# Kernel tuning notes

Hardware: AMD Instinct MI355X
Metric: run time of the kernel (lower is better)

The kernel has to match this reference:

```python
import jax, jax.numpy as jnp
import numpy as np

B = 64        # number of graph segments
BASE = 384    # mean verts per segment
LMAX = 512    # pad length (counts in [256, 512])
H_DIM = 256
H_DIV = 128   # h_dim // h_dim_div
HEADS = 4
DH = H_DIV // HEADS  # 32


def _counts(seed):
    rng = np.random.default_rng(seed)
    d = rng.integers(-128, 129, B)
    d[1::2] = -d[::2]            # paired so the total is exactly B*BASE
    return (BASE + d).astype(np.int64)


def _pad_indices(counts, L):
    # Gather indices/mask mapping packed ragged tokens -> padded [B, L].
    counts = np.asarray(counts)
    off = np.concatenate([[0], np.cumsum(counts)[:-1]])
    ar = np.arange(L)[None, :]
    mask = ar < counts[:, None]
    idx = np.where(mask, off[:, None] + ar, 0)
    return idx, mask


def setup_inputs() -> dict:
    key = jax.random.key(0)
    ks = jax.random.split(key, 16)
    src_num_verts = _counts(0)
    dst_num_verts = _counts(1)
    total = B * BASE  # 24576 for both src and dst

    def w(k, shape):
        return 0.02 * jax.random.normal(k, shape, jnp.float32)

    return {
        'src_h': jax.random.normal(ks[0], (total, H_DIM), jnp.float32),
        'dst_h': jax.random.normal(ks[1], (total, H_DIM), jnp.float32),
        'src_num_verts': src_num_verts,
        'dst_num_verts': dst_num_verts,
        # 1x1 Conv1d == linear over channels
        'Wq': w(ks[2], (H_DIV, H_DIM)), 'bq': w(ks[3], (H_DIV,)),
        'Wk': w(ks[4], (H_DIV, H_DIM)), 'bk': w(ks[5], (H_DIV,)),
        'Wv': w(ks[6], (H_DIV, H_DIM)), 'bv': w(ks[7], (H_DIV,)),
        'Wm': w(ks[8], (H_DIV, H_DIV)), 'bm': w(ks[9], (H_DIV,)),
        'W1': w(ks[10], (H_DIM, H_DIM + H_DIV)), 'b1': w(ks[11], (H_DIM,)),
        'g1': 1.0 + 0.1 * jax.random.normal(ks[12], (H_DIM,), jnp.float32),
        'be1': w(ks[13], (H_DIM,)),
        'rm1': w(ks[14], (H_DIM,)),
        'rv1': jax.random.uniform(ks[15], (H_DIM,), jnp.float32, 0.5, 1.5),
        'W2': w(jax.random.fold_in(key, 100), (H_DIM, H_DIM)),
        'b2': w(jax.random.fold_in(key, 101), (H_DIM,)),
        'g2': 1.0 + 0.1 * jax.random.normal(jax.random.fold_in(key, 102), (H_DIM,), jnp.float32),
        'be2': w(jax.random.fold_in(key, 103), (H_DIM,)),
        'rm2': w(jax.random.fold_in(key, 104), (H_DIM,)),
        'rv2': jax.random.uniform(jax.random.fold_in(key, 105), (H_DIM,), jnp.float32, 0.5, 1.5),
    }


def _bn(x, g, b, rm, rv):
    # BatchNorm1d in eval mode (running stats)
    return (x - rm) / jnp.sqrt(rv + 1e-5) * g + b


def reference(src_h, dst_h, src_num_verts, dst_num_verts,
              Wq, bq, Wk, bk, Wv, bv, Wm, bm,
              W1, b1, g1, be1, rm1, rv1,
              W2, b2, g2, be2, rm2, rv2):
    didx, dmask = _pad_indices(dst_num_verts, LMAX)
    sidx, smask = _pad_indices(src_num_verts, LMAX)

    # fused projections over all packed tokens (1x1 conv == matmul)
    q = src_h_proj = dst_h @ Wq.T + bq        # [Nd, H_DIV]
    k = src_h @ Wk.T + bk                     # [Ns, H_DIV]
    v = src_h @ Wv.T + bv

    # pad to block-diagonal batched form; channel c = d*HEADS + h per torch view
    qp = q[didx].reshape(B, LMAX, DH, HEADS)
    kp = k[sidx].reshape(B, LMAX, DH, HEADS)
    vp = v[sidx].reshape(B, LMAX, DH, HEADS)

    scores = jnp.einsum('bndh,bmdh->bhnm', qp, kp) / (DH ** 0.5)
    scores = jnp.where(jnp.asarray(smask)[:, None, None, :], scores, -1e9)
    attn = jax.nn.softmax(scores, axis=-1)
    msg = jnp.einsum('bhnm,bmdh->bndh', attn, vp).reshape(B, LMAX, H_DIV)
    msg = msg @ Wm.T + bm                     # merge conv

    bb, ii = np.nonzero(dmask)                # unpad back to packed layout
    h_msg = msg[bb, ii]                       # [Nd, H_DIV]

    x = jnp.concatenate([dst_h, h_msg], axis=-1)
    x = _bn(x @ W1.T + b1, g1, be1, rm1, rv1)
    x = jax.nn.relu(x)
    x = _bn(x @ W2.T + b2, g2, be2, rm2, rv2)
    return dst_h + x
```

## Files before the change

kernel.cpp:

```cpp
#include <hip/hip_runtime.h>
#include <hip/hip_bf16.h>
#include <math.h>

#define B_SEG 64
#define HDIM 256
#define HDIV 128
#define NHEADS 4
#define DH 32
#define QSC 0.17677669529663687f

typedef unsigned short u16;
typedef unsigned int u32;

typedef __attribute__((ext_vector_type(8))) short s8v;
typedef __attribute__((ext_vector_type(4))) short s4v;
typedef __attribute__((ext_vector_type(4))) float f4v;

#if defined(__HIP_DEVICE_COMPILE__)
#if __has_builtin(__builtin_amdgcn_mfma_f32_16x16x16_bf16)
#define MFMA16(a, b, c) __builtin_amdgcn_mfma_f32_16x16x16_bf16(a, b, c, 0, 0, 0)
#elif __has_builtin(__builtin_amdgcn_mfma_f32_16x16x16bf16_1k)
#define MFMA16(a, b, c) __builtin_amdgcn_mfma_f32_16x16x16bf16_1k(a, b, c, 0, 0, 0)
#else
#error "no 16x16x16 bf16 mfma builtin on device"
#endif
#else
#define MFMA16(a, b, c) (c)
#endif

__device__ __forceinline__ u16 f2bf(float f) {
    u32 v;
    __builtin_memcpy(&v, &f, 4);
    u32 r = v + 0x7fffu + ((v >> 16) & 1u);
    return (u16)(r >> 16);
}

__device__ __forceinline__ void async_cp16(const u16* g, u16* l) {
    __builtin_amdgcn_global_load_lds(
        (const __attribute__((address_space(1))) u32*)g,
        (__attribute__((address_space(3))) u32*)l, 16, 0, 0);
}

__global__ __launch_bounds__(256) void k_prep(
    const float* __restrict__ Wq, const float* __restrict__ bq,
    const float* __restrict__ Wk, const float* __restrict__ bk,
    const float* __restrict__ Wv, const float* __restrict__ bv,
    const float* __restrict__ Wm, const float* __restrict__ bm,
    const float* __restrict__ W1, const float* __restrict__ b1,
    const float* __restrict__ g1, const float* __restrict__ be1,
    const float* __restrict__ rm1, const float* __restrict__ rv1,
    const float* __restrict__ W2, const float* __restrict__ b2,
    const float* __restrict__ g2, const float* __restrict__ be2,
    const float* __restrict__ rm2, const float* __restrict__ rv2,
    const int* __restrict__ sc_raw, const int* __restrict__ dc_raw,
    const float* __restrict__ src_h, const float* __restrict__ dst_h,
    int* __restrict__ meta,
    u16* __restrict__ pWq, u16* __restrict__ pWkv,
    u16* __restrict__ pW1f, u16* __restrict__ pW2,
    float* __restrict__ bqp, float* __restrict__ bkvp,
    float* __restrict__ sc1, float* __restrict__ sh1,
    float* __restrict__ sc2, float* __restrict__ sh2,
    u16* __restrict__ srcb, u16* __restrict__ dstb, int ntot) {
    if (blockIdx.x < 1028) {
        int idx = blockIdx.x * 256 + threadIdx.x;
        if (idx < 32768) {
            int cp = idx >> 8, k = idx & 255;
            int c = ((cp & 31) << 2) | (cp >> 5);
            pWq[idx] = f2bf(Wq[c * 256 + k]);
        } else if (idx < 98304) {
            int i = idx - 32768;
            int rp = i >> 8, k = i & 255;
            int r = rp & 127;
            int c = ((r & 31) << 2) | (r >> 5);
            float v = (rp < 128) ? Wk[c * 256 + k] : Wv[c * 256 + k];
            pWkv[i] = f2bf(v);
        } else if (idx < 163840) {
            int i = idx - 98304;
            int o = i >> 8, k = i & 255;
            pW1f[o * 384 + k] = f2bf(W1[o * 384 + k]);
        } else if (idx < 196608) {
            int i = idx - 163840;
            int o = i >> 7, cp = i & 127;
            int c = ((cp & 31) << 2) | (cp >> 5);
            float acc = 0.f;
            for (int j = 0; j < 128; j++)
                acc += W1[o * 384 + 256 + j] * Wm[j * 128 + c];
            pW1f[o * 384 + 256 + cp] = f2bf(acc);
        } else if (idx < 262144) {
            int i = idx - 196608;
            pW2[i] = f2bf(W2[i]);
        } else if (idx < 263168) {
            int p = idx - 262144;
            if (p < 128) {
                int c = ((p & 31) << 2) | (p >> 5);
                bqp[p] = bq[c] * QSC;
            } else if (p < 384) {
                int r = p - 128; int rr = r & 127;
                int c = ((rr & 31) << 2) | (rr >> 5);
                bkvp[r] = (r < 128) ? bk[c] : bv[c];
            } else if (p < 640) {
                int o = p - 384;
                float bsum = 0.f;
                for (int j = 0; j < 128; j++)
                    bsum += W1[o * 384 + 256 + j] * bm[j];
                float s = g1[o] * rsqrtf(rv1[o] + 1e-5f);
                sc1[o] = s;
                sh1[o] = (b1[o] + bsum - rm1[o]) * s + be1[o];
            } else if (p < 896) {
                int o = p - 640;
                float s = g2[o] * rsqrtf(rv2[o] + 1e-5f);
                sc2[o] = s;
                sh2[o] = (b2[o] - rm2[o]) * s + be2[o];
            }
        }
    } else if (blockIdx.x == 1028) {
        if (threadIdx.x == 0) {
            bool is64 = (sc_raw[1] == 0);
            int so = 0, dofs = 0;
            for (int i = 0; i < B_SEG; i++) {
                int s = is64 ? sc_raw[2 * i] : sc_raw[i];
                int d = is64 ? dc_raw[2 * i] : dc_raw[i];
                meta[i] = s; meta[64 + i] = d;
                meta[128 + i] = so; meta[192 + i] = dofs;
                so += s; dofs += d;
            }
        }
    } else {
        int i = (blockIdx.x - 1029) * 256 + threadIdx.x;
        int half = ntot * 64;
        const float4* s;
        u16* o;
        int j = i;
        if (i < half) { s = (const float4*)src_h; o = srcb; }
        else { s = (const float4*)dst_h; o = dstb; j = i - half; }
        float4 v = s[j];
        ushort4 u = {f2bf(v.x), f2bf(v.y), f2bf(v.z), f2bf(v.w)};
        ((ushort4*)o)[j] = u;
    }
}

__device__ __forceinline__ void gemm_body(
    const u16* __restrict__ A, int lda,
    const u16* __restrict__ A2, int lda2, int K1,
    const u16* __restrict__ Bw, int K, int m0, int n0,
    const float* __restrict__ scale, const float* __restrict__ shift,
    const float* __restrict__ resid,
    void* __restrict__ Cout, int ldc, int flags,
    u16* Al, u16* Bl) {
    int tid = threadIdx.x;
    int w = tid >> 6, lane = tid & 63;
    int wm = w & 1, wn = w >> 1;
    int l15 = lane & 15, quad = lane >> 4;
    int srow = w * 32 + (lane >> 2);
    int scol = (lane & 3) << 3;
    u16* al0 = Al + w * 1024;
    u16* bl0 = Bl + w * 1024;
    f4v acc[4][4] = {};

    for (int k0 = 0; k0 < K; k0 += 32) {
        const u16* Ag; int aL, acol;
        if (k0 < K1) { Ag = A; aL = lda; acol = k0; }
        else { Ag = A2; aL = lda2; acol = k0 - K1; }
        async_cp16(&Ag[(size_t)(m0 + srow) * aL + acol + scol], al0);
        async_cp16(&Ag[(size_t)(m0 + srow + 16) * aL + acol + scol], al0 + 512);
        async_cp16(&Bw[(size_t)(n0 + srow) * K + k0 + scol], bl0);
        async_cp16(&Bw[(size_t)(n0 + srow + 16) * K + k0 + scol], bl0 + 512);
        __syncthreads();
        s8v af[4], bf[4];
#pragma unroll
        for (int i = 0; i < 4; i++)
            af[i] = *(const s8v*)(&Al[(wm * 64 + i * 16 + l15) * 32 + quad * 8]);
#pragma unroll
        for (int j = 0; j < 4; j++)
            bf[j] = *(const s8v*)(&Bl[(wn * 64 + j * 16 + l15) * 32 + quad * 8]);
#pragma unroll
        for (int i = 0; i < 4; i++)
#pragma unroll
            for (int j = 0; j < 4; j++)
                acc[i][j] = __builtin_amdgcn_mfma_f32_16x16x32_bf16(
                    af[i], bf[j], acc[i][j], 0, 0, 0);
        __syncthreads();
    }
#pragma unroll
    for (int i = 0; i < 4; i++) {
#pragma unroll
        for (int j = 0; j < 4; j++) {
            int n = n0 + wn * 64 + j * 16 + l15;
            float sc = scale ? scale[n] : 1.f;
            float sh = shift ? shift[n] : 0.f;
#pragma unroll
            for (int r = 0; r < 4; r++) {
                int m = m0 + wm * 64 + i * 16 + quad * 4 + r;
                float v = acc[i][j][r];
                if (flags & 4) v *= QSC;
                v = v * sc + sh;
                if (flags & 1) v = fmaxf(v, 0.f);
                if (resid) v += resid[(size_t)m * 256 + n];
                if (flags & 2) ((float*)Cout)[(size_t)m * ldc + n] = v;
                else ((u16*)Cout)[(size_t)m * ldc + n] = f2bf(v);
            }
        }
    }
}

__global__ __launch_bounds__(256) void k_qkv(
    const u16* __restrict__ dstb, const u16* __restrict__ srcb,
    const u16* __restrict__ pWq, const u16* __restrict__ pWkv,
    const float* __restrict__ bqp, const float* __restrict__ bkvp,
    u16* __restrict__ qb, u16* __restrict__ kvb) {
    __shared__ u16 Al[4096];
    __shared__ u16 Bl[4096];
    int m0 = blockIdx.x * 128;
    if (blockIdx.y == 0)
        gemm_body(dstb, 256, dstb, 256, 256, pWq, 256, m0, 0,
                  nullptr, bqp, nullptr, qb, 128, 4, Al, Bl);
    else
        gemm_body(srcb, 256, srcb, 256, 256, pWkv, 256, m0, (blockIdx.y - 1) * 128,
                  nullptr, bkvp, nullptr, kvb, 256, 0, Al, Bl);
}

__global__ __launch_bounds__(256, 4) void k_mlp(
    const u16* __restrict__ dstb, const u16* __restrict__ msgb,
    const u16* __restrict__ pW1f, const u16* __restrict__ pW2,
    const float* __restrict__ sc1, const float* __restrict__ sh1,
    const float* __restrict__ sc2, const float* __restrict__ sh2,
    const float* __restrict__ dst_h, float* __restrict__ out) {
    __shared__ u16 Al[32 * 32];
    __shared__ u16 Bl[256 * 32];
    __shared__ u16 X1[32 * 256];
    int m0 = blockIdx.x * 32;
    int tid = threadIdx.x;
    int w = tid >> 6, lane = tid & 63;
    int l15 = lane & 15, quad = lane >> 4;
    int srow = lane >> 2;
    int scol = (lane & 3) << 3;
    f4v acc[2][4];

#pragma unroll
    for (int i = 0; i < 2; i++)
#pragma unroll
        for (int j = 0; j < 4; j++) acc[i][j] = (f4v){0.f, 0.f, 0.f, 0.f};

    for (int k0 = 0; k0 < 384; k0 += 32) {
        const u16* Ag; int aL, acol;
        if (k0 < 256) { Ag = dstb; aL = 256; acol = k0; }
        else { Ag = msgb; aL = 128; acol = k0 - 256; }
#pragma unroll
        for (int q = 0; q < 4; q++)
            async_cp16(&pW1f[(size_t)(w * 64 + q * 16 + srow) * 384 + k0 + scol],
                       Bl + (w * 64 + q * 16) * 32);
        if (w < 2)
            async_cp16(&Ag[(size_t)(m0 + w * 16 + srow) * aL + acol + scol],
                       Al + w * 16 * 32);
        __syncthreads();
        s8v af[2], bf[4];
#pragma unroll
        for (int i = 0; i < 2; i++)
            af[i] = *(const s8v*)(&Al[(i * 16 + l15) * 32 + quad * 8]);
#pragma unroll
        for (int j = 0; j < 4; j++)
            bf[j] = *(const s8v*)(&Bl[(w * 64 + j * 16 + l15) * 32 + quad * 8]);
#pragma unroll
        for (int i = 0; i < 2; i++)
#pragma unroll
            for (int j = 0; j < 4; j++)
                acc[i][j] = __builtin_amdgcn_mfma_f32_16x16x32_bf16(
                    af[i], bf[j], acc[i][j], 0, 0, 0);
        __syncthreads();
    }
#pragma unroll
    for (int i = 0; i < 2; i++) {
#pragma unroll
        for (int j = 0; j < 4; j++) {
            int n = w * 64 + j * 16 + l15;
            float sc = sc1[n], sh = sh1[n];
#pragma unroll
            for (int r = 0; r < 4; r++) {
                int row = i * 16 + quad * 4 + r;
                float v = fmaxf(acc[i][j][r] * sc + sh, 0.f);
                X1[row * 256 + ((n >> 3) ^ (row & 7)) * 8 + (n & 7)] = f2bf(v);
            }
        }
    }
    __syncthreads();

#pragma unroll
    for (int i = 0; i < 2; i++)
#pragma unroll
        for (int j = 0; j < 4; j++) acc[i][j] = (f4v){0.f, 0.f, 0.f, 0.f};

    for (int k0 = 0; k0 < 256; k0 += 32) {
#pragma unroll
        for (int q = 0; q < 4; q++)
            async_cp16(&pW2[(size_t)(w * 64 + q * 16 + srow) * 256 + k0 + scol],
                       Bl + (w * 64 + q * 16) * 32);
        __syncthreads();
        s8v af[2], bf[4];
#pragma unroll
        for (int i = 0; i < 2; i++) {
            int row = i * 16 + l15;
            af[i] = *(const s8v*)(
                &X1[row * 256 + (((k0 >> 3) + quad) ^ (row & 7)) * 8]);
        }
#pragma unroll
        for (int j = 0; j < 4; j++)
            bf[j] = *(const s8v*)(&Bl[(w * 64 + j * 16 + l15) * 32 + quad * 8]);
#pragma unroll
        for (int i = 0; i < 2; i++)
#pragma unroll
            for (int j = 0; j < 4; j++)
                acc[i][j] = __builtin_amdgcn_mfma_f32_16x16x32_bf16(
                    af[i], bf[j], acc[i][j], 0, 0, 0);
        __syncthreads();
    }
#pragma unroll
    for (int i = 0; i < 2; i++) {
#pragma unroll
        for (int j = 0; j < 4; j++) {
            int n = w * 64 + j * 16 + l15;
            float sc = sc2[n], sh = sh2[n];
#pragma unroll
            for (int r = 0; r < 4; r++) {
                int m = m0 + i * 16 + quad * 4 + r;
                float v = acc[i][j][r] * sc + sh + dst_h[(size_t)m * 256 + n];
                out[(size_t)m * 256 + n] = v;
            }
        }
    }
}

__global__ __launch_bounds__(512, 4) void k_attn(
    const u16* __restrict__ qb, const u16* __restrict__ kvb,
    const int* __restrict__ meta, u16* __restrict__ msgb) {
    extern __shared__ u16 sm[];
    u16* Kl = sm;
    u16* Vl = sm + 16384;
    int b = blockIdx.x, h = blockIdx.y, z = blockIdx.z;
    int ns = meta[b], nd = meta[64 + b];
    int soff = meta[128 + b], doff = meta[192 + b];
    int tid = threadIdx.x, w = tid >> 6, lane = tid & 63;
    int l15 = lane & 15, quad = lane >> 4;

    {
        int m = tid;
        if (m < ns) {
            const uint4* ks = (const uint4*)&kvb[(size_t)(soff + m) * 256 + h * 32];
#pragma unroll
            for (int s = 0; s < 4; s++)
                *(uint4*)&Kl[m * 32 + (s ^ ((m >> 1) & 3)) * 8] = ks[s];
            uint4 vv[4];
            const uint4* vs =
                (const uint4*)&kvb[(size_t)(soff + m) * 256 + 128 + h * 32];
#pragma unroll
            for (int s = 0; s < 4; s++) vv[s] = vs[s];
            const u16* pv = (const u16*)vv;
#pragma unroll
            for (int d = 0; d < 32; d++)
                Vl[d * 512 + ((m >> 3) ^ (d & 7)) * 8 + (m & 7)] = pv[d];
        } else {
#pragma unroll
            for (int d = 0; d < 32; d++)
                Vl[d * 512 + ((m >> 3) ^ (d & 7)) * 8 + (m & 7)] = 0;
        }
    }
    __syncthreads();

    int nc32 = (ns + 31) >> 5;
    int ksw = (quad ^ ((l15 >> 1) & 3)) * 8;
    int vsw = l15 & 7;
    int half4 = (quad & 1) * 4;
    const u16* VlLo = Vl + l15 * 512;
    const u16* VlHi = Vl + (16 + l15) * 512;

    for (int s0 = (z * 8 + w) * 16; s0 < nd; s0 += 256) {
        int qr = min(s0 + l15, nd - 1);
        s8v aq = *(const s8v*)&qb[(size_t)(doff + qr) * 128 + h * 32 + quad * 8];

        f4v oa0 = {0.f, 0.f, 0.f, 0.f};
        f4v oa1 = {0.f, 0.f, 0.f, 0.f};
        float lsum = 0.f;
        for (int c = 0; c < nc32; c++) {
            int kr0 = c * 32 + l15;
            s8v bk0 = *(const s8v*)&Kl[kr0 * 32 + ksw];
            s8v bk1 = *(const s8v*)&Kl[(kr0 + 16) * 32 + ksw];
            f4v sa = __builtin_amdgcn_mfma_f32_16x16x32_bf16(
                bk0, aq, (f4v){0.f, 0.f, 0.f, 0.f}, 0, 0, 0);
            f4v sb = __builtin_amdgcn_mfma_f32_16x16x32_bf16(
                bk1, aq, (f4v){0.f, 0.f, 0.f, 0.f}, 0, 0, 0);
            int kb = c * 32 + quad * 4;
            float e0[4], e1[4];
#pragma unroll
            for (int r = 0; r < 4; r++) {
                float va = (kb + r < ns) ? __expf(sa[r]) : 0.f;
                float vb = (kb + 16 + r < ns) ? __expf(sb[r]) : 0.f;
                e0[r] = va; e1[r] = vb;
                lsum += va + vb;
            }
            union { s4v v; u32 u[2]; } pb0, pb1;
            pb0.u[0] = (u32)f2bf(e0[0]) | ((u32)f2bf(e0[1]) << 16);
            pb0.u[1] = (u32)f2bf(e0[2]) | ((u32)f2bf(e0[3]) << 16);
            pb1.u[0] = (u32)f2bf(e1[0]) | ((u32)f2bf(e1[1]) << 16);
            pb1.u[1] = (u32)f2bf(e1[2]) | ((u32)f2bf(e1[3]) << 16);
            int slb = c * 4 + (quad >> 1);
            s4v v00 = *(const s4v*)&VlLo[(slb ^ vsw) * 8 + half4];
            s4v v01 = *(const s4v*)&VlLo[((slb + 2) ^ vsw) * 8 + half4];
            s4v v10 = *(const s4v*)&VlHi[(slb ^ vsw) * 8 + half4];
            s4v v11 = *(const s4v*)&VlHi[((slb + 2) ^ vsw) * 8 + half4];
            oa0 = MFMA16(v00, pb0.v, oa0);
            oa0 = MFMA16(v01, pb1.v, oa0);
            oa1 = MFMA16(v10, pb0.v, oa1);
            oa1 = MFMA16(v11, pb1.v, oa1);
        }
        lsum += __shfl_xor(lsum, 16, 64);
        lsum += __shfl_xor(lsum, 32, 64);
        float inv = 1.f / lsum;
        int row = s0 + l15;
        if (row < nd) {
            size_t base = (size_t)(doff + row) * 128 + h * 32;
            ushort4 o0 = {f2bf(oa0[0] * inv), f2bf(oa0[1] * inv),
                          f2bf(oa0[2] * inv), f2bf(oa0[3] * inv)};
            ushort4 o1 = {f2bf(oa1[0] * inv), f2bf(oa1[1] * inv),
                          f2bf(oa1[2] * inv), f2bf(oa1[3] * inv)};
            *(ushort4*)&msgb[base + quad * 4] = o0;
            *(ushort4*)&msgb[base + 16 + quad * 4] = o1;
        }
    }
}

extern "C" void kernel_launch(void* const* d_in, const int* in_sizes, int n_in,
                              void* d_out, int out_size, void* d_ws, size_t ws_size,
                              hipStream_t stream) {
    const float* src_h = (const float*)d_in[0];
    const float* dst_h = (const float*)d_in[1];
    const int* snv = (const int*)d_in[2];
    const int* dnv = (const int*)d_in[3];
    const float* Wq = (const float*)d_in[4];  const float* bq = (const float*)d_in[5];
    const float* Wk = (const float*)d_in[6];  const float* bk = (const float*)d_in[7];
    const float* Wv = (const float*)d_in[8];  const float* bv = (const float*)d_in[9];
    const float* Wm = (const float*)d_in[10]; const float* bm = (const float*)d_in[11];
    const float* W1 = (const float*)d_in[12]; const float* b1 = (const float*)d_in[13];
    const float* g1 = (const float*)d_in[14]; const float* be1 = (const float*)d_in[15];
    const float* rm1 = (const float*)d_in[16]; const float* rv1 = (const float*)d_in[17];
    const float* W2 = (const float*)d_in[18]; const float* b2 = (const float*)d_in[19];
    const float* g2 = (const float*)d_in[20]; const float* be2 = (const float*)d_in[21];
    const float* rm2 = (const float*)d_in[22]; const float* rv2 = (const float*)d_in[23];

    int ntot = out_size / HDIM;
    int mt = ntot / 128;

    char* ws = (char*)d_ws;
    int* meta = (int*)ws;
    float* bqp = (float*)(ws + 4096);
    float* bkvp = (float*)(ws + 4608);
    float* sc1 = (float*)(ws + 6144);
    float* sh1 = (float*)(ws + 7168);
    float* sc2 = (float*)(ws + 8192);
    float* sh2 = (float*)(ws + 9216);
    u16* pWq = (u16*)(ws + 16384);
    u16* pWkv = (u16*)(ws + 81920);
    u16* pW1f = (u16*)(ws + 212992);
    u16* pW2 = (u16*)(ws + 409600);
    u16* srcb = (u16*)(ws + 1048576);
    u16* dstb = (u16*)(ws + 13631488);
    u16* msgb = (u16*)(ws + 26214400);

    u16* qb = (u16*)d_out;
    u16* kvb = qb + (size_t)ntot * 128;

    (void)hipFuncSetAttribute((const void*)k_attn,
                              hipFuncAttributeMaxDynamicSharedMemorySize, 65536);

    k_prep<<<dim3(1029 + ntot / 2), dim3(256), 0, stream>>>(
        Wq, bq, Wk, bk, Wv, bv, Wm, bm, W1, b1, g1, be1, rm1, rv1,
        W2, b2, g2, be2, rm2, rv2, snv, dnv, src_h, dst_h, meta,
        pWq, pWkv, pW1f, pW2, bqp, bkvp, sc1, sh1, sc2, sh2,
        srcb, dstb, ntot);
    k_qkv<<<dim3(mt, 3), dim3(256), 0, stream>>>(
        dstb, srcb, pWq, pWkv, bqp, bkvp, qb, kvb);
    k_attn<<<dim3(B_SEG, NHEADS, 2), dim3(512), 65536, stream>>>(
        qb, kvb, meta, msgb);
    k_mlp<<<dim3(ntot / 32), dim3(256), 0, stream>>>(
        dstb, msgb, pW1f, pW2, sc1, sh1, sc2, sh2, dst_h, (float*)d_out);
}
```

Before: 203.2 us.

## Double-buffer LDS tiles in the QKV and MLP GEMM loops

Adds ping-pong shared-memory buffers to the QKV projection GEMM and to both GEMM phases of the fused MLP kernel. The next K-slice is issued with async copies before the MFMAs on the current slice, so global-load latency can overlap with compute, and one barrier per iteration is removed. The first W2 slice is also prefetched while the first layer's epilogue runs. In exchange, LDS use grows, to about 52KB per block in k_mlp, which may lower the number of resident blocks below the requested 4.

Result: no change. 201.2 us (-1.0%).

```diff
diff --git a/kernel.cpp b/kernel.cpp
--- a/kernel.cpp
+++ b/kernel.cpp
@@ -153,26 +153,34 @@
     int l15 = lane & 15, quad = lane >> 4;
     int srow = w * 32 + (lane >> 2);
     int scol = (lane & 3) << 3;
-    u16* al0 = Al + w * 1024;
-    u16* bl0 = Bl + w * 1024;
     f4v acc[4][4] = {};
 
-    for (int k0 = 0; k0 < K; k0 += 32) {
+    auto STAGE = [&](int buf, int k0) {
         const u16* Ag; int aL, acol;
         if (k0 < K1) { Ag = A; aL = lda; acol = k0; }
         else { Ag = A2; aL = lda2; acol = k0 - K1; }
+        u16* al0 = Al + buf * 4096 + w * 1024;
+        u16* bl0 = Bl + buf * 4096 + w * 1024;
         async_cp16(&Ag[(size_t)(m0 + srow) * aL + acol + scol], al0);
         async_cp16(&Ag[(size_t)(m0 + srow + 16) * aL + acol + scol], al0 + 512);
         async_cp16(&Bw[(size_t)(n0 + srow) * K + k0 + scol], bl0);
         async_cp16(&Bw[(size_t)(n0 + srow + 16) * K + k0 + scol], bl0 + 512);
-        __syncthreads();
+    };
+
+    STAGE(0, 0);
+    __syncthreads();
+    int cur = 0;
+    for (int k0 = 0; k0 < K; k0 += 32) {
+        if (k0 + 32 < K) STAGE(cur ^ 1, k0 + 32);
+        const u16* Ab = Al + cur * 4096;
+        const u16* Bb = Bl + cur * 4096;
         s8v af[4], bf[4];
 #pragma unroll
         for (int i = 0; i < 4; i++)
-            af[i] = *(const s8v*)(&Al[(wm * 64 + i * 16 + l15) * 32 + quad * 8]);
+            af[i] = *(const s8v*)(&Ab[(wm * 64 + i * 16 + l15) * 32 + quad * 8]);
 #pragma unroll
         for (int j = 0; j < 4; j++)
-            bf[j] = *(const s8v*)(&Bl[(wn * 64 + j * 16 + l15) * 32 + quad * 8]);
+            bf[j] = *(const s8v*)(&Bb[(wn * 64 + j * 16 + l15) * 32 + quad * 8]);
 #pragma unroll
         for (int i = 0; i < 4; i++)
 #pragma unroll
@@ -180,6 +188,7 @@
                 acc[i][j] = __builtin_amdgcn_mfma_f32_16x16x32_bf16(
                     af[i], bf[j], acc[i][j], 0, 0, 0);
         __syncthreads();
+        cur ^= 1;
     }
 #pragma unroll
     for (int i = 0; i < 4; i++) {
@@ -208,8 +217,8 @@
     const u16* __restrict__ pWq, const u16* __restrict__ pWkv,
     const float* __restrict__ bqp, const float* __restrict__ bkvp,
     u16* __restrict__ qb, u16* __restrict__ kvb) {
-    __shared__ u16 Al[4096];
-    __shared__ u16 Bl[4096];
+    __shared__ u16 Al[8192];
+    __shared__ u16 Bl[8192];
     int m0 = blockIdx.x * 128;
     if (blockIdx.y == 0)
         gemm_body(dstb, 256, dstb, 256, 256, pWq, 256, m0, 0,
@@ -225,8 +234,8 @@
     const float* __restrict__ sc1, const float* __restrict__ sh1,
     const float* __restrict__ sc2, const float* __restrict__ sh2,
     const float* __restrict__ dst_h, float* __restrict__ out) {
-    __shared__ u16 Al[32 * 32];
-    __shared__ u16 Bl[256 * 32];
+    __shared__ u16 Al[2048];
+    __shared__ u16 Bl[16384];
     __shared__ u16 X1[32 * 256];
     int m0 = blockIdx.x * 32;
     int tid = threadIdx.x;
@@ -236,30 +245,44 @@
     int scol = (lane & 3) << 3;
     f4v acc[2][4];
 
-#pragma unroll
-    for (int i = 0; i < 2; i++)
-#pragma unroll
-        for (int j = 0; j < 4; j++) acc[i][j] = (f4v){0.f, 0.f, 0.f, 0.f};
-
-    for (int k0 = 0; k0 < 384; k0 += 32) {
+    auto STAGE1 = [&](int buf, int k0) {
         const u16* Ag; int aL, acol;
         if (k0 < 256) { Ag = dstb; aL = 256; acol = k0; }
         else { Ag = msgb; aL = 128; acol = k0 - 256; }
 #pragma unroll
         for (int q = 0; q < 4; q++)
             async_cp16(&pW1f[(size_t)(w * 64 + q * 16 + srow) * 384 + k0 + scol],
-                       Bl + (w * 64 + q * 16) * 32);
+                       Bl + buf * 8192 + (w * 64 + q * 16) * 32);
         if (w < 2)
             async_cp16(&Ag[(size_t)(m0 + w * 16 + srow) * aL + acol + scol],
-                       Al + w * 16 * 32);
-        __syncthreads();
+                       Al + buf * 1024 + w * 16 * 32);
+    };
+    auto STAGE2 = [&](int buf, int k0) {
+#pragma unroll
+        for (int q = 0; q < 4; q++)
+            async_cp16(&pW2[(size_t)(w * 64 + q * 16 + srow) * 256 + k0 + scol],
+                       Bl + buf * 8192 + (w * 64 + q * 16) * 32);
+    };
+
+#pragma unroll
+    for (int i = 0; i < 2; i++)
+#pragma unroll
+        for (int j = 0; j < 4; j++) acc[i][j] = (f4v){0.f, 0.f, 0.f, 0.f};
+
+    STAGE1(0, 0);
+    __syncthreads();
+    int cur = 0;
+    for (int k0 = 0; k0 < 384; k0 += 32) {
+        if (k0 + 32 < 384) STAGE1(cur ^ 1, k0 + 32);
+        const u16* Ab = Al + cur * 1024;
+        const u16* Bb = Bl + cur * 8192;
         s8v af[2], bf[4];
 #pragma unroll
         for (int i = 0; i < 2; i++)
-            af[i] = *(const s8v*)(&Al[(i * 16 + l15) * 32 + quad * 8]);
+            af[i] = *(const s8v*)(&Ab[(i * 16 + l15) * 32 + quad * 8]);
 #pragma unroll
         for (int j = 0; j < 4; j++)
-            bf[j] = *(const s8v*)(&Bl[(w * 64 + j * 16 + l15) * 32 + quad * 8]);
+            bf[j] = *(const s8v*)(&Bb[(w * 64 + j * 16 + l15) * 32 + quad * 8]);
 #pragma unroll
         for (int i = 0; i < 2; i++)
 #pragma unroll
@@ -267,7 +290,10 @@
                 acc[i][j] = __builtin_amdgcn_mfma_f32_16x16x32_bf16(
                     af[i], bf[j], acc[i][j], 0, 0, 0);
         __syncthreads();
-    }
+        cur ^= 1;
+    }
+
+    STAGE2(0, 0);
 #pragma unroll
     for (int i = 0; i < 2; i++) {
 #pragma unroll
@@ -289,12 +315,10 @@
 #pragma unroll
         for (int j = 0; j < 4; j++) acc[i][j] = (f4v){0.f, 0.f, 0.f, 0.f};
 
+    cur = 0;
     for (int k0 = 0; k0 < 256; k0 += 32) {
-#pragma unroll
-        for (int q = 0; q < 4; q++)
-            async_cp16(&pW2[(size_t)(w * 64 + q * 16 + srow) * 256 + k0 + scol],
-                       Bl + (w * 64 + q * 16) * 32);
-        __syncthreads();
+        if (k0 + 32 < 256) STAGE2(cur ^ 1, k0 + 32);
+        const u16* Bb = Bl + cur * 8192;
         s8v af[2], bf[4];
 #pragma unroll
         for (int i = 0; i < 2; i++) {
@@ -304,7 +328,7 @@
         }
 #pragma unroll
         for (int j = 0; j < 4; j++)
-            bf[j] = *(const s8v*)(&Bl[(w * 64 + j * 16 + l15) * 32 + quad * 8]);
+            bf[j] = *(const s8v*)(&Bb[(w * 64 + j * 16 + l15) * 32 + quad * 8]);
 #pragma unroll
         for (int i = 0; i < 2; i++)
 #pragma unroll
@@ -312,6 +336,7 @@
                 acc[i][j] = __builtin_amdgcn_mfma_f32_16x16x32_bf16(
                     af[i], bf[j], acc[i][j], 0, 0, 0);
         __syncthreads();
+        cur ^= 1;
     }
 #pragma unroll
     for (int i = 0; i < 2; i++) {
```
